# Kernel optimization log

Measured on AMD Instinct MI355X. Metric: run time of the kernel, lower is better.

The kernel has to match this reference:

```python
import jax, jax.numpy as jnp
import numpy as np
from jax import lax

# fixed differential-operator kernel bank K() from SPDE_pac (8 channels of 3x3 stencils)
_K = np.zeros((8, 3, 3), np.float32)
_K[0, 1, 1] = 1.0
_K[1, 1, 1] = 2.0
_K[2, 1, 0] = -1.0; _K[2, 1, 2] = -1.0
_K[3, 1, 1] = 2.0
_K[4, 0, 1] = -1.0; _K[4, 2, 1] = -1.0
_K[5, 0, 0] = -0.5; _K[5, 2, 2] = -0.5; _K[5, 0, 2] = 0.5; _K[5, 2, 0] = 0.5
_K[6, 1, 0] = -1.0; _K[6, 1, 2] = 1.0
_K[7, 0, 1] = 1.0; _K[7, 2, 1] = -1.0
_KMAT = jnp.asarray(_K)


def _conv(x, w):
    # 3x3 same-padded conv, no bias (torch Conv2d padding=1, bias=False)
    return lax.conv_general_dilated(x, w, (1, 1), 'SAME',
                                    dimension_numbers=('NCHW', 'OIHW', 'NCHW'))


def _softplus10(x):
    return jax.nn.softplus(10.0 * x) / 10.0


def _forward(x, conv1_w, conv2_w, conv3_w, pac_w, pac_b):
    b, t, h, w = x.shape
    # ---- encode_param_CNN ----
    p = _conv(jax.nn.relu(x), conv1_w)
    p = _conv(jax.nn.relu(p), conv2_w)
    params = _conv(p, conv3_w)                       # [b, 6t, h, w]
    # ---- decode_param_CNN (kept in [b,t,h,w] layout; H = gamma*I + v v^T per pixel) ----
    kappa = _softplus10(params[:, :t])
    m1d = params[:, t:2 * t]                         # decoder m1 -> m[:,0]
    m2d = params[:, 2 * t:3 * t]                     # decoder m2 -> m[:,1]
    gamma = _softplus10(params[:, 3 * t:4 * t])
    vx = params[:, 4 * t:5 * t]
    vy = params[:, 5 * t:6 * t]
    H11 = gamma + vx * vx
    H22 = gamma + vy * vy
    H12 = vx * vy
    # ---- SPDE_pac kernel construction ----
    # guide channels as in source: (kappa, H11, 1/H11, H22, 1/H22, H12, m[:,1], m[:,0])
    guide = jnp.stack([kappa, H11, 1.0 / H11, H22, 1.0 / H22, H12, m2d, m1d], axis=2)  # [b,t,8,h,w]
    w_ker = jnp.einsum('ide,btihw->btdehw', _KMAT, guide)   # [b,t,3,3,h,w]
    w_ker = w_ker.at[:, :, 1, 1].add(1.0)                   # w_I identity-center kernel
    # ---- pixel-adaptive conv; loop over k is independent (reads x[:,k+1]) -> vectorize over time ----
    xin = x[:, 1:]                                          # [b,t-1,h,w]
    xp = jnp.pad(xin, ((0, 0), (0, 0), (1, 1), (1, 1)))
    patches = jnp.stack([xp[:, :, d:d + h, e:e + w]
                         for d in range(3) for e in range(3)], axis=2)  # [b,t-1,9,h,w]
    wflat = w_ker[:, 1:].reshape(b, t - 1, 9, h, w)
    out = jnp.einsum('k,btkhw,btkhw->bthw', pac_w.reshape(9), wflat, patches) + pac_b[0]
    # last time slice of x_spde is never written -> zeros
    return jnp.concatenate([out, jnp.zeros((b, 1, h, w), x.dtype)], axis=1)


def setup_inputs() -> dict:
    key = jax.random.key(0)
    ks = jax.random.split(key, 6)
    b, t, h, w = 4, 10, 256, 256
    dim_ae = 32
    x = jax.random.normal(ks[0], (b, t, h, w), jnp.float32)
    conv1_w = jax.random.normal(ks[1], (dim_ae, t, 3, 3), jnp.float32) * 0.05
    conv2_w = jax.random.normal(ks[2], (2 * dim_ae, dim_ae, 3, 3), jnp.float32) * 0.05
    conv3_w = jax.random.normal(ks[3], (6 * t, 2 * dim_ae, 3, 3), jnp.float32) * 0.05
    pac_w = jax.random.normal(ks[4], (1, 1, 3, 3), jnp.float32) * 0.2
    pac_b = jax.random.normal(ks[5], (1,), jnp.float32) * 0.1
    return {"x": x, "conv1_w": conv1_w, "conv2_w": conv2_w,
            "conv3_w": conv3_w, "pac_w": pac_w, "pac_b": pac_b}


def reference(x, conv1_w, conv2_w, conv3_w, pac_w, pac_b):
    return _forward(x, conv1_w, conv2_w, conv3_w, pac_w, pac_b)
```

## Files before the change

### kernel.cpp

```cpp
#include <hip/hip_runtime.h>
#include <math.h>

#define HH 256
#define WW 256
#define HW (HH * WW)
#define TB 10
#define PSTR 260

typedef __attribute__((ext_vector_type(4))) float f32x4;
typedef __attribute__((ext_vector_type(8))) short s16x8;

__device__ __forceinline__ float sp10(float x) {
    float z = 10.0f * x;
    return (fmaxf(z, 0.0f) + log1pf(expf(-fabsf(z)))) * 0.1f;
}

__device__ __forceinline__ unsigned short f2bf(float f) {
    unsigned u = __float_as_uint(f);
    u = u + 0x7FFFu + ((u >> 16) & 1u);
    return (unsigned short)(u >> 16);
}
__device__ __forceinline__ void bsplit(float v, unsigned short& h, unsigned short& l) {
    h = f2bf(v);
    float hf = __uint_as_float(((unsigned)h) << 16);
    l = f2bf(v - hf);
}
__device__ __forceinline__ unsigned pk(unsigned short a, unsigned short b) {
    return (unsigned)a | ((unsigned)b << 16);
}
__device__ __forceinline__ void sp2(float a, float b, unsigned& uh, unsigned& ul) {
    unsigned short h1, l1, h2, l2;
    bsplit(a, h1, l1); bsplit(b, h2, l2);
    uh = pk(h1, h2); ul = pk(l1, l2);
}

__global__ __launch_bounds__(256) void prep_weights(
    const float* __restrict__ w1, const float* __restrict__ w2,
    const float* __restrict__ w3,
    float* __restrict__ wt1,
    unsigned short* __restrict__ wA2h, unsigned short* __restrict__ wA2l,
    unsigned short* __restrict__ wA3h, unsigned short* __restrict__ wA3l)
{
    int idx = blockIdx.x * 256 + threadIdx.x;
    if (idx < 2880) {
        int ci = idx / 288; int rem = idx - ci * 288;
        int tap = rem / 32; int co = rem - tap * 32;
        wt1[idx] = w1[co * 90 + ci * 9 + tap];
    }
    if (idx < 18432) {
        int t = idx / 2048; int rem = idx - t * 2048;
        int co = rem >> 5; int ci = rem & 31;
        unsigned short h, l;
        bsplit(w2[(co * 32 + ci) * 9 + t], h, l);
        wA2h[idx] = h; wA2l[idx] = l;
    }
    if (idx < 36864) {
        int t = idx / 4096; int rem = idx - t * 4096;
        int co = rem >> 6; int ci = rem & 63;
        float v = 0.0f;
        if (co < 54) {
            int tt = co / 6 + 1;
            int g  = co - (tt - 1) * 6;
            v = w3[((g * 10 + tt) * 64 + ci) * 9 + t];
        }
        unsigned short h, l;
        bsplit(v, h, l);
        wA3h[idx] = h; wA3l[idx] = l;
    }
}

__global__ __launch_bounds__(256, 4) void conv1_k(
    const float* __restrict__ x, const float* __restrict__ wt1,
    unsigned short* __restrict__ q1h, unsigned short* __restrict__ q1l)
{
    __shared__ float tile[10 * 612];
    const int tx = threadIdx.x & 15, ty = threadIdx.x >> 4;
    const int h0 = blockIdx.y * 32, w0 = blockIdx.x * 16;
    const int b = blockIdx.z;
    const float* inb = x + (size_t)b * TB * HW;

    float acc0[32], acc1[32];
#pragma unroll
    for (int c = 0; c < 32; ++c) { acc0[c] = 0.0f; acc1[c] = 0.0f; }

    for (int i = threadIdx.x; i < 10 * 612; i += 256) {
        int ci = i / 612; int r = i - ci * 612;
        int row = r / 18; int col = r - row * 18;
        int gy = h0 + row - 1, gx = w0 + col - 1;
        float v = 0.0f;
        if (gy >= 0 && gy < HH && gx >= 0 && gx < WW)
            v = fmaxf(inb[(size_t)ci * HW + gy * WW + gx], 0.0f);
        tile[i] = v;
    }
    __syncthreads();

    for (int ci = 0; ci < 10; ++ci) {
        const float* tp = &tile[ci * 612 + (2 * ty) * 18 + tx];
        float v[12];
#pragma unroll
        for (int r = 0; r < 4; ++r)
#pragma unroll
            for (int c = 0; c < 3; ++c)
                v[r * 3 + c] = tp[r * 18 + c];
        const float* wp = wt1 + ci * 288;
#pragma unroll
        for (int t = 0; t < 9; ++t) {
            float a0 = v[t], a1 = v[t + 3];
#pragma unroll
            for (int c = 0; c < 32; ++c) {
                float wv = wp[t * 32 + c];
                acc0[c] = fmaf(wv, a0, acc0[c]);
                acc1[c] = fmaf(wv, a1, acc1[c]);
            }
        }
    }

    const int h = h0 + 2 * ty, w = w0 + tx;
    const size_t q1base = (size_t)b * HW * 32;
#pragma unroll
    for (int p = 0; p < 2; ++p) {
        const float* src = p ? acc1 : acc0;
        size_t off = q1base + ((size_t)(h + p) * WW + w) * 32;
#pragma unroll
        for (int g = 0; g < 4; ++g) {
            uint4 Uh, Ul;
            sp2(fmaxf(src[g*8+0],0.f), fmaxf(src[g*8+1],0.f), Uh.x, Ul.x);
            sp2(fmaxf(src[g*8+2],0.f), fmaxf(src[g*8+3],0.f), Uh.y, Ul.y);
            sp2(fmaxf(src[g*8+4],0.f), fmaxf(src[g*8+5],0.f), Uh.z, Ul.z);
            sp2(fmaxf(src[g*8+6],0.f), fmaxf(src[g*8+7],0.f), Uh.w, Ul.w);
            *(uint4*)(q1h + off + g * 8) = Uh;
            *(uint4*)(q1l + off + g * 8) = Ul;
        }
    }
}

__global__ __launch_bounds__(256, 3) void conv2_mfma(
    const unsigned short* __restrict__ q1h, const unsigned short* __restrict__ q1l,
    const unsigned short* __restrict__ wA2h, const unsigned short* __restrict__ wA2l,
    unsigned short* __restrict__ q2h, unsigned short* __restrict__ q2l)
{
    __shared__ short lds[324 * 72];
    const int tid = threadIdx.x;
    const int lane = tid & 63, wave = tid >> 6;
    const int px = lane & 15, quad = lane >> 4;
    const int h0 = blockIdx.y * 16, w0 = blockIdx.x * 16, b = blockIdx.z;

    f32x4 acc[4][4];
#pragma unroll
    for (int r = 0; r < 4; ++r)
#pragma unroll
        for (int ct = 0; ct < 4; ++ct)
            acc[r][ct] = (f32x4){0.f, 0.f, 0.f, 0.f};

    for (int i = tid; i < 648; i += 256) {
        int plane = (i >= 324) ? 1 : 0;
        int pos = i - plane * 324;
        int row = pos / 18, col = pos - (pos / 18) * 18;
        int gy = h0 + row - 1, gx = w0 + col - 1;
        uint4 v0 = {0,0,0,0}, v1 = v0, v2 = v0, v3 = v0;
        if (gy >= 0 && gy < HH && gx >= 0 && gx < WW) {
            const uint4* gp = (const uint4*)((plane ? q1l : q1h)
                + (size_t)b * HW * 32 + ((size_t)gy * WW + gx) * 32);
            v0 = gp[0]; v1 = gp[1]; v2 = gp[2]; v3 = gp[3];
        }
        uint4* dp = (uint4*)&lds[pos * 72 + plane * 32];
        dp[0] = v0; dp[1] = v1; dp[2] = v2; dp[3] = v3;
    }
    __syncthreads();

#pragma unroll
    for (int t = 0; t < 9; ++t) {
        const int dy = t / 3, dx = t - 3 * (t / 3);
#pragma unroll
        for (int ctp = 0; ctp < 2; ++ctp) {
            const int c0 = ctp * 2;
            int wb0 = (t * 64 + (c0 + 0) * 16 + px) * 32 + quad * 8;
            int wb1 = (t * 64 + (c0 + 1) * 16 + px) * 32 + quad * 8;
            s16x8 ah0 = *(const s16x8*)(wA2h + wb0);
            s16x8 ah1 = *(const s16x8*)(wA2h + wb1);
            s16x8 al0 = *(const s16x8*)(wA2l + wb0);
            s16x8 al1 = *(const s16x8*)(wA2l + wb1);
#pragma unroll
            for (int r = 0; r < 4; ++r) {
                int py = wave * 4 + r;
                const short* bp = &lds[((py + dy) * 18 + (px + dx)) * 72 + quad * 8];
                s16x8 bh = *(const s16x8*)bp;
                s16x8 bl = *(const s16x8*)(bp + 32);
                acc[r][c0+0] = __builtin_amdgcn_mfma_f32_16x16x32_bf16(ah0, bh, acc[r][c0+0], 0, 0, 0);
                acc[r][c0+0] = __builtin_amdgcn_mfma_f32_16x16x32_bf16(al0, bh, acc[r][c0+0], 0, 0, 0);
                acc[r][c0+0] = __builtin_amdgcn_mfma_f32_16x16x32_bf16(ah0, bl, acc[r][c0+0], 0, 0, 0);
                acc[r][c0+1] = __builtin_amdgcn_mfma_f32_16x16x32_bf16(ah1, bh, acc[r][c0+1], 0, 0, 0);
                acc[r][c0+1] = __builtin_amdgcn_mfma_f32_16x16x32_bf16(al1, bh, acc[r][c0+1], 0, 0, 0);
                acc[r][c0+1] = __builtin_amdgcn_mfma_f32_16x16x32_bf16(ah1, bl, acc[r][c0+1], 0, 0, 0);
            }
        }
    }

#pragma unroll
    for (int r = 0; r < 4; ++r) {
        int py = wave * 4 + r;
        size_t pix = (size_t)b * HW + (size_t)(h0 + py) * WW + (w0 + px);
#pragma unroll
        for (int ct = 0; ct < 4; ++ct) {
            int co0 = ct * 16 + quad * 4;
            uint2 Uh, Ul;
            sp2(acc[r][ct][0], acc[r][ct][1], Uh.x, Ul.x);
            sp2(acc[r][ct][2], acc[r][ct][3], Uh.y, Ul.y);
            size_t off = pix * 64 + co0;
            *(uint2*)(q2h + off) = Uh;
            *(uint2*)(q2l + off) = Ul;
        }
    }
}

__global__ __launch_bounds__(256, 3) void conv3_mfma(
    const unsigned short* __restrict__ q2h, const unsigned short* __restrict__ q2l,
    const unsigned short* __restrict__ wA3h, const unsigned short* __restrict__ wA3l,
    const float* __restrict__ x, const float* __restrict__ pacw,
    const float* __restrict__ pacb, float* __restrict__ out)
{
    __shared__ short lds[324 * 72];
    float* smemf = (float*)lds;
    const int tid = threadIdx.x;
    const int lane = tid & 63, wave = tid >> 6;
    const int px = lane & 15, quad = lane >> 4;
    const int h0 = blockIdx.y * 16, w0 = blockIdx.x * 16, b = blockIdx.z;

    f32x4 acc[4][4];
#pragma unroll
    for (int r = 0; r < 4; ++r)
#pragma unroll
        for (int ct = 0; ct < 4; ++ct)
            acc[r][ct] = (f32x4){0.f, 0.f, 0.f, 0.f};

#pragma unroll
    for (int half = 0; half < 2; ++half) {
        if (half) __syncthreads();
        for (int i = tid; i < 648; i += 256) {
            int plane = (i >= 324) ? 1 : 0;
            int pos = i - plane * 324;
            int row = pos / 18, col = pos - (pos / 18) * 18;
            int gy = h0 + row - 1, gx = w0 + col - 1;
            uint4 v0 = {0,0,0,0}, v1 = v0, v2 = v0, v3 = v0;
            if (gy >= 0 && gy < HH && gx >= 0 && gx < WW) {
                const uint4* gp = (const uint4*)((plane ? q2l : q2h)
                    + (size_t)b * HW * 64 + ((size_t)gy * WW + gx) * 64 + half * 32);
                v0 = gp[0]; v1 = gp[1]; v2 = gp[2]; v3 = gp[3];
            }
            uint4* dp = (uint4*)&lds[pos * 72 + plane * 32];
            dp[0] = v0; dp[1] = v1; dp[2] = v2; dp[3] = v3;
        }
        __syncthreads();

#pragma unroll
        for (int t = 0; t < 9; ++t) {
            const int dy = t / 3, dx = t - 3 * (t / 3);
#pragma unroll
            for (int ctp = 0; ctp < 2; ++ctp) {
                const int c0 = ctp * 2;
                int wb0 = (t * 64 + (c0 + 0) * 16 + px) * 64 + half * 32 + quad * 8;
                int wb1 = (t * 64 + (c0 + 1) * 16 + px) * 64 + half * 32 + quad * 8;
                s16x8 ah0 = *(const s16x8*)(wA3h + wb0);
                s16x8 ah1 = *(const s16x8*)(wA3h + wb1);
                s16x8 al0 = *(const s16x8*)(wA3l + wb0);
                s16x8 al1 = *(const s16x8*)(wA3l + wb1);
#pragma unroll
                for (int r = 0; r < 4; ++r) {
                    int py = wave * 4 + r;
                    const short* bp = &lds[((py + dy) * 18 + (px + dx)) * 72 + quad * 8];
                    s16x8 bh = *(const s16x8*)bp;
                    s16x8 bl = *(const s16x8*)(bp + 32);
                    acc[r][c0+0] = __builtin_amdgcn_mfma_f32_16x16x32_bf16(ah0, bh, acc[r][c0+0], 0, 0, 0);
                    acc[r][c0+0] = __builtin_amdgcn_mfma_f32_16x16x32_bf16(al0, bh, acc[r][c0+0], 0, 0, 0);
                    acc[r][c0+0] = __builtin_amdgcn_mfma_f32_16x16x32_bf16(ah0, bl, acc[r][c0+0], 0, 0, 0);
                    acc[r][c0+1] = __builtin_amdgcn_mfma_f32_16x16x32_bf16(ah1, bh, acc[r][c0+1], 0, 0, 0);
                    acc[r][c0+1] = __builtin_amdgcn_mfma_f32_16x16x32_bf16(al1, bh, acc[r][c0+1], 0, 0, 0);
                    acc[r][c0+1] = __builtin_amdgcn_mfma_f32_16x16x32_bf16(ah1, bl, acc[r][c0+1], 0, 0, 0);
                }
            }
        }
    }

    float pw[9];
#pragma unroll
    for (int k = 0; k < 9; ++k) pw[k] = pacw[k];
    const float pbias = pacb[0];
    const int h = h0 + (tid >> 4), w = w0 + (tid & 15);
    const float* xb = x + (size_t)b * TB * HW;
    float* ob = out + (size_t)b * TB * HW;

#pragma unroll
    for (int chunk = 0; chunk < 2; ++chunk) {
        const int lo = chunk * 30, hi = chunk ? 54 : 30;
        __syncthreads();
#pragma unroll
        for (int r = 0; r < 4; ++r) {
            int pfr = (wave * 4 + r) * 16 + px;
#pragma unroll
            for (int ct = 0; ct < 4; ++ct)
#pragma unroll
                for (int g = 0; g < 4; ++g) {
                    int co = ct * 16 + quad * 4 + g;
                    if (co >= lo && co < hi)
                        smemf[(co - lo) * PSTR + pfr] = acc[r][ct][g];
                }
        }
        __syncthreads();

        const int j0 = chunk * 5, j1 = chunk ? 9 : 5;
        for (int j = j0; j < j1; ++j) {
            const int cb = j * 6 - lo;
            float kappa = sp10(smemf[(cb + 0) * PSTR + tid]);
            float m1d   = smemf[(cb + 1) * PSTR + tid];
            float m2d   = smemf[(cb + 2) * PSTR + tid];
            float gamma = sp10(smemf[(cb + 3) * PSTR + tid]);
            float vx    = smemf[(cb + 4) * PSTR + tid];
            float vy    = smemf[(cb + 5) * PSTR + tid];
            float H11 = gamma + vx * vx;
            float H22 = gamma + vy * vy;
            float H12 = vx * vy;
            float iH11 = 1.0f / H11;
            float iH22 = 1.0f / H22;
            float wk[9];
            wk[0] = -0.5f * H12;  wk[1] = -iH22 + m1d;  wk[2] = 0.5f * H12;
            wk[3] = -iH11 - m2d;
            wk[4] = kappa + 2.0f * H11 + 2.0f * H22 + 1.0f;
            wk[5] = -iH11 + m2d;
            wk[6] = 0.5f * H12;   wk[7] = -iH22 - m1d;  wk[8] = -0.5f * H12;

            const float* xc = xb + (size_t)(j + 1) * HW;
            float s = 0.0f;
#pragma unroll
            for (int dy = 0; dy < 3; ++dy)
#pragma unroll
                for (int dx = 0; dx < 3; ++dx) {
                    int gy = h + dy - 1, gx = w + dx - 1;
                    float xv = (gy >= 0 && gy < HH && gx >= 0 && gx < WW)
                                   ? xc[gy * WW + gx] : 0.0f;
                    s = fmaf(pw[dy * 3 + dx] * wk[dy * 3 + dx], xv, s);
                }
            ob[(size_t)j * HW + (size_t)h * WW + w] = s + pbias;
        }
    }
    ob[(size_t)9 * HW + (size_t)h * WW + w] = 0.0f;
}

extern "C" void kernel_launch(void* const* d_in, const int* in_sizes, int n_in,
                              void* d_out, int out_size, void* d_ws, size_t ws_size,
                              hipStream_t stream)
{
    const float* x    = (const float*)d_in[0];
    const float* w1   = (const float*)d_in[1];
    const float* w2   = (const float*)d_in[2];
    const float* w3   = (const float*)d_in[3];
    const float* pacw = (const float*)d_in[4];
    const float* pacb = (const float*)d_in[5];
    float* out = (float*)d_out;
    char* p = (char*)d_ws;

    float* wt1 = (float*)p;
    unsigned short* wA2h = (unsigned short*)(p + 11520);
    unsigned short* wA2l = (unsigned short*)(p + 11520 + 36864);
    unsigned short* wA3h = (unsigned short*)(p + 11520 + 2 * 36864);
    unsigned short* wA3l = (unsigned short*)(p + 11520 + 2 * 36864 + 73728);
    const size_t woff = 11520 + 2 * 36864 + 2 * 73728;

    prep_weights<<<144, 256, 0, stream>>>(w1, w2, w3, wt1, wA2h, wA2l, wA3h, wA3l);

    const size_t q1sz1 = (size_t)HW * 32 * 2;
    const size_t q2sz1 = (size_t)HW * 64 * 2;
    const size_t need_full = woff + 4 * (2 * q1sz1 + 2 * q2sz1);
    dim3 blk(256);

    if (ws_size >= need_full) {
        unsigned short* q1h = (unsigned short*)(p + woff);
        unsigned short* q1l = (unsigned short*)(p + woff + 4 * q1sz1);
        unsigned short* q2h = (unsigned short*)(p + woff + 8 * q1sz1);
        unsigned short* q2l = (unsigned short*)(p + woff + 8 * q1sz1 + 4 * q2sz1);
        conv1_k<<<dim3(16, 8, 4), blk, 0, stream>>>(x, wt1, q1h, q1l);
        conv2_mfma<<<dim3(16, 16, 4), blk, 0, stream>>>(q1h, q1l, wA2h, wA2l, q2h, q2l);
        conv3_mfma<<<dim3(16, 16, 4), blk, 0, stream>>>(q2h, q2l, wA3h, wA3l,
                                                        x, pacw, pacb, out);
    } else {
        unsigned short* q1h = (unsigned short*)(p + woff);
        unsigned short* q1l = (unsigned short*)(p + woff + q1sz1);
        unsigned short* q2h = (unsigned short*)(p + woff + 2 * q1sz1);
        unsigned short* q2l = (unsigned short*)(p + woff + 2 * q1sz1 + q2sz1);
        for (int b = 0; b < 4; ++b) {
            const float* xb = x + (size_t)b * TB * HW;
            float* outb = out + (size_t)b * TB * HW;
            conv1_k<<<dim3(16, 8, 1), blk, 0, stream>>>(xb, wt1, q1h, q1l);
            conv2_mfma<<<dim3(16, 16, 1), blk, 0, stream>>>(q1h, q1l, wA2h, wA2l, q2h, q2l);
            conv3_mfma<<<dim3(16, 16, 1), blk, 0, stream>>>(q2h, q2l, wA3h, wA3l,
                                                            xb, pacw, pacb, outb);
        }
    }
}
```

Before: 310.0 us.

## Split conv2/conv3 output channels across 8 waves with 512-thread blocks

```diff
diff --git a/kernel.cpp b/kernel.cpp
--- a/kernel.cpp
+++ b/kernel.cpp
@@ -134,7 +134,7 @@
     }
 }
 
-__global__ __launch_bounds__(256, 3) void conv2_mfma(
+__global__ __launch_bounds__(512, 4) void conv2_mfma(
     const unsigned short* __restrict__ q1h, const unsigned short* __restrict__ q1l,
     const unsigned short* __restrict__ wA2h, const unsigned short* __restrict__ wA2l,
     unsigned short* __restrict__ q2h, unsigned short* __restrict__ q2l)
@@ -142,17 +142,18 @@
     __shared__ short lds[324 * 72];
     const int tid = threadIdx.x;
     const int lane = tid & 63, wave = tid >> 6;
+    const int wq = wave & 3, wc = wave >> 2;
     const int px = lane & 15, quad = lane >> 4;
     const int h0 = blockIdx.y * 16, w0 = blockIdx.x * 16, b = blockIdx.z;
 
-    f32x4 acc[4][4];
+    f32x4 acc[4][2];
 #pragma unroll
     for (int r = 0; r < 4; ++r)
 #pragma unroll
-        for (int ct = 0; ct < 4; ++ct)
-            acc[r][ct] = (f32x4){0.f, 0.f, 0.f, 0.f};
-
-    for (int i = tid; i < 648; i += 256) {
+        for (int c = 0; c < 2; ++c)
+            acc[r][c] = (f32x4){0.f, 0.f, 0.f, 0.f};
+
+    for (int i = tid; i < 648; i += 512) {
         int plane = (i >= 324) ? 1 : 0;
         int pos = i - plane * 324;
         int row = pos / 18, col = pos - (pos / 18) * 18;
@@ -171,41 +172,38 @@
 #pragma unroll
     for (int t = 0; t < 9; ++t) {
         const int dy = t / 3, dx = t - 3 * (t / 3);
-#pragma unroll
-        for (int ctp = 0; ctp < 2; ++ctp) {
-            const int c0 = ctp * 2;
-            int wb0 = (t * 64 + (c0 + 0) * 16 + px) * 32 + quad * 8;
-            int wb1 = (t * 64 + (c0 + 1) * 16 + px) * 32 + quad * 8;
-            s16x8 ah0 = *(const s16x8*)(wA2h + wb0);
-            s16x8 ah1 = *(const s16x8*)(wA2h + wb1);
-            s16x8 al0 = *(const s16x8*)(wA2l + wb0);
-            s16x8 al1 = *(const s16x8*)(wA2l + wb1);
-#pragma unroll
-            for (int r = 0; r < 4; ++r) {
-                int py = wave * 4 + r;
-                const short* bp = &lds[((py + dy) * 18 + (px + dx)) * 72 + quad * 8];
-                s16x8 bh = *(const s16x8*)bp;
-                s16x8 bl = *(const s16x8*)(bp + 32);
-                acc[r][c0+0] = __builtin_amdgcn_mfma_f32_16x16x32_bf16(ah0, bh, acc[r][c0+0], 0, 0, 0);
-                acc[r][c0+0] = __builtin_amdgcn_mfma_f32_16x16x32_bf16(al0, bh, acc[r][c0+0], 0, 0, 0);
-                acc[r][c0+0] = __builtin_amdgcn_mfma_f32_16x16x32_bf16(ah0, bl, acc[r][c0+0], 0, 0, 0);
-                acc[r][c0+1] = __builtin_amdgcn_mfma_f32_16x16x32_bf16(ah1, bh, acc[r][c0+1], 0, 0, 0);
-                acc[r][c0+1] = __builtin_amdgcn_mfma_f32_16x16x32_bf16(al1, bh, acc[r][c0+1], 0, 0, 0);
-                acc[r][c0+1] = __builtin_amdgcn_mfma_f32_16x16x32_bf16(ah1, bl, acc[r][c0+1], 0, 0, 0);
-            }
+        const int ct0 = wc * 2;
+        int wb0 = (t * 64 + (ct0 + 0) * 16 + px) * 32 + quad * 8;
+        int wb1 = (t * 64 + (ct0 + 1) * 16 + px) * 32 + quad * 8;
+        s16x8 ah0 = *(const s16x8*)(wA2h + wb0);
+        s16x8 ah1 = *(const s16x8*)(wA2h + wb1);
+        s16x8 al0 = *(const s16x8*)(wA2l + wb0);
+        s16x8 al1 = *(const s16x8*)(wA2l + wb1);
+#pragma unroll
+        for (int r = 0; r < 4; ++r) {
+            int py = wq * 4 + r;
+            const short* bp = &lds[((py + dy) * 18 + (px + dx)) * 72 + quad * 8];
+            s16x8 bh = *(const s16x8*)bp;
+            s16x8 bl = *(const s16x8*)(bp + 32);
+            acc[r][0] = __builtin_amdgcn_mfma_f32_16x16x32_bf16(ah0, bh, acc[r][0], 0, 0, 0);
+            acc[r][0] = __builtin_amdgcn_mfma_f32_16x16x32_bf16(al0, bh, acc[r][0], 0, 0, 0);
+            acc[r][0] = __builtin_amdgcn_mfma_f32_16x16x32_bf16(ah0, bl, acc[r][0], 0, 0, 0);
+            acc[r][1] = __builtin_amdgcn_mfma_f32_16x16x32_bf16(ah1, bh, acc[r][1], 0, 0, 0);
+            acc[r][1] = __builtin_amdgcn_mfma_f32_16x16x32_bf16(al1, bh, acc[r][1], 0, 0, 0);
+            acc[r][1] = __builtin_amdgcn_mfma_f32_16x16x32_bf16(ah1, bl, acc[r][1], 0, 0, 0);
         }
     }
 
 #pragma unroll
     for (int r = 0; r < 4; ++r) {
-        int py = wave * 4 + r;
+        int py = wq * 4 + r;
         size_t pix = (size_t)b * HW + (size_t)(h0 + py) * WW + (w0 + px);
 #pragma unroll
-        for (int ct = 0; ct < 4; ++ct) {
-            int co0 = ct * 16 + quad * 4;
+        for (int c = 0; c < 2; ++c) {
+            int co0 = (wc * 2 + c) * 16 + quad * 4;
             uint2 Uh, Ul;
-            sp2(acc[r][ct][0], acc[r][ct][1], Uh.x, Ul.x);
-            sp2(acc[r][ct][2], acc[r][ct][3], Uh.y, Ul.y);
+            sp2(acc[r][c][0], acc[r][c][1], Uh.x, Ul.x);
+            sp2(acc[r][c][2], acc[r][c][3], Uh.y, Ul.y);
             size_t off = pix * 64 + co0;
             *(uint2*)(q2h + off) = Uh;
             *(uint2*)(q2l + off) = Ul;
@@ -213,7 +211,7 @@
     }
 }
 
-__global__ __launch_bounds__(256, 3) void conv3_mfma(
+__global__ __launch_bounds__(512, 4) void conv3_mfma(
     const unsigned short* __restrict__ q2h, const unsigned short* __restrict__ q2l,
     const unsigned short* __restrict__ wA3h, const unsigned short* __restrict__ wA3l,
     const float* __restrict__ x, const float* __restrict__ pacw,
@@ -223,20 +221,21 @@
     float* smemf = (float*)lds;
     const int tid = threadIdx.x;
     const int lane = tid & 63, wave = tid >> 6;
+    const int wq = wave & 3, wc = wave >> 2;
     const int px = lane & 15, quad = lane >> 4;
     const int h0 = blockIdx.y * 16, w0 = blockIdx.x * 16, b = blockIdx.z;
 
-    f32x4 acc[4][4];
+    f32x4 acc[4][2];
 #pragma unroll
     for (int r = 0; r < 4; ++r)
 #pragma unroll
-        for (int ct = 0; ct < 4; ++ct)
-            acc[r][ct] = (f32x4){0.f, 0.f, 0.f, 0.f};
+        for (int c = 0; c < 2; ++c)
+            acc[r][c] = (f32x4){0.f, 0.f, 0.f, 0.f};
 
 #pragma unroll
     for (int half = 0; half < 2; ++half) {
         if (half) __syncthreads();
-        for (int i = tid; i < 648; i += 256) {
+        for (int i = tid; i < 648; i += 512) {
             int plane = (i >= 324) ? 1 : 0;
             int pos = i - plane * 324;
             int row = pos / 18, col = pos - (pos / 18) * 18;
@@ -255,28 +254,25 @@
 #pragma unroll
         for (int t = 0; t < 9; ++t) {
             const int dy = t / 3, dx = t - 3 * (t / 3);
-#pragma unroll
-            for (int ctp = 0; ctp < 2; ++ctp) {
-                const int c0 = ctp * 2;
-                int wb0 = (t * 64 + (c0 + 0) * 16 + px) * 64 + half * 32 + quad * 8;
-                int wb1 = (t * 64 + (c0 + 1) * 16 + px) * 64 + half * 32 + quad * 8;
-                s16x8 ah0 = *(const s16x8*)(wA3h + wb0);
-                s16x8 ah1 = *(const s16x8*)(wA3h + wb1);
-                s16x8 al0 = *(const s16x8*)(wA3l + wb0);
-                s16x8 al1 = *(const s16x8*)(wA3l + wb1);
-#pragma unroll
-                for (int r = 0; r < 4; ++r) {
-                    int py = wave * 4 + r;
-                    const short* bp = &lds[((py + dy) * 18 + (px + dx)) * 72 + quad * 8];
-                    s16x8 bh = *(const s16x8*)bp;
-                    s16x8 bl = *(const s16x8*)(bp + 32);
-                    acc[r][c0+0] = __builtin_amdgcn_mfma_f32_16x16x32_bf16(ah0, bh, acc[r][c0+0], 0, 0, 0);
-                    acc[r][c0+0] = __builtin_amdgcn_mfma_f32_16x16x32_bf16(al0, bh, acc[r][c0+0], 0, 0, 0);
-                    acc[r][c0+0] = __builtin_amdgcn_mfma_f32_16x16x32_bf16(ah0, bl, acc[r][c0+0], 0, 0, 0);
-                    acc[r][c0+1] = __builtin_amdgcn_mfma_f32_16x16x32_bf16(ah1, bh, acc[r][c0+1], 0, 0, 0);
-                    acc[r][c0+1] = __builtin_amdgcn_mfma_f32_16x16x32_bf16(al1, bh, acc[r][c0+1], 0, 0, 0);
-                    acc[r][c0+1] = __builtin_amdgcn_mfma_f32_16x16x32_bf16(ah1, bl, acc[r][c0+1], 0, 0, 0);
-                }
+            const int ct0 = wc * 2;
+            int wb0 = (t * 64 + (ct0 + 0) * 16 + px) * 64 + half * 32 + quad * 8;
+            int wb1 = (t * 64 + (ct0 + 1) * 16 + px) * 64 + half * 32 + quad * 8;
+            s16x8 ah0 = *(const s16x8*)(wA3h + wb0);
+            s16x8 ah1 = *(const s16x8*)(wA3h + wb1);
+            s16x8 al0 = *(const s16x8*)(wA3l + wb0);
+            s16x8 al1 = *(const s16x8*)(wA3l + wb1);
+#pragma unroll
+            for (int r = 0; r < 4; ++r) {
+                int py = wq * 4 + r;
+                const short* bp = &lds[((py + dy) * 18 + (px + dx)) * 72 + quad * 8];
+                s16x8 bh = *(const s16x8*)bp;
+                s16x8 bl = *(const s16x8*)(bp + 32);
+                acc[r][0] = __builtin_amdgcn_mfma_f32_16x16x32_bf16(ah0, bh, acc[r][0], 0, 0, 0);
+                acc[r][0] = __builtin_amdgcn_mfma_f32_16x16x32_bf16(al0, bh, acc[r][0], 0, 0, 0);
+                acc[r][0] = __builtin_amdgcn_mfma_f32_16x16x32_bf16(ah0, bl, acc[r][0], 0, 0, 0);
+                acc[r][1] = __builtin_amdgcn_mfma_f32_16x16x32_bf16(ah1, bh, acc[r][1], 0, 0, 0);
+                acc[r][1] = __builtin_amdgcn_mfma_f32_16x16x32_bf16(al1, bh, acc[r][1], 0, 0, 0);
+                acc[r][1] = __builtin_amdgcn_mfma_f32_16x16x32_bf16(ah1, bl, acc[r][1], 0, 0, 0);
             }
         }
     }
@@ -285,7 +281,9 @@
 #pragma unroll
     for (int k = 0; k < 9; ++k) pw[k] = pacw[k];
     const float pbias = pacb[0];
-    const int h = h0 + (tid >> 4), w = w0 + (tid & 15);
+    const int grp = tid >> 8;
+    const int pidx = tid & 255;
+    const int h = h0 + (pidx >> 4), w = w0 + (pidx & 15);
     const float* xb = x + (size_t)b * TB * HW;
     float* ob = out + (size_t)b * TB * HW;
 
@@ -295,27 +293,28 @@
         __syncthreads();
 #pragma unroll
         for (int r = 0; r < 4; ++r) {
-            int pfr = (wave * 4 + r) * 16 + px;
-#pragma unroll
-            for (int ct = 0; ct < 4; ++ct)
+            int pfr = (wq * 4 + r) * 16 + px;
+#pragma unroll
+            for (int c = 0; c < 2; ++c)
 #pragma unroll
                 for (int g = 0; g < 4; ++g) {
-                    int co = ct * 16 + quad * 4 + g;
+                    int co = (wc * 2 + c) * 16 + quad * 4 + g;
                     if (co >= lo && co < hi)
-                        smemf[(co - lo) * PSTR + pfr] = acc[r][ct][g];
+                        smemf[(co - lo) * PSTR + pfr] = acc[r][c][g];
                 }
         }
         __syncthreads();
 
-        const int j0 = chunk * 5, j1 = chunk ? 9 : 5;
+        const int j0 = chunk ? (grp ? 7 : 5) : (grp ? 3 : 0);
+        const int j1 = chunk ? (grp ? 9 : 7) : (grp ? 5 : 3);
         for (int j = j0; j < j1; ++j) {
             const int cb = j * 6 - lo;
-            float kappa = sp10(smemf[(cb + 0) * PSTR + tid]);
-            float m1d   = smemf[(cb + 1) * PSTR + tid];
-            float m2d   = smemf[(cb + 2) * PSTR + tid];
-            float gamma = sp10(smemf[(cb + 3) * PSTR + tid]);
-            float vx    = smemf[(cb + 4) * PSTR + tid];
-            float vy    = smemf[(cb + 5) * PSTR + tid];
+            float kappa = sp10(smemf[(cb + 0) * PSTR + pidx]);
+            float m1d   = smemf[(cb + 1) * PSTR + pidx];
+            float m2d   = smemf[(cb + 2) * PSTR + pidx];
+            float gamma = sp10(smemf[(cb + 3) * PSTR + pidx]);
+            float vx    = smemf[(cb + 4) * PSTR + pidx];
+            float vy    = smemf[(cb + 5) * PSTR + pidx];
             float H11 = gamma + vx * vx;
             float H22 = gamma + vy * vy;
             float H12 = vx * vy;
@@ -342,7 +341,8 @@
             ob[(size_t)j * HW + (size_t)h * WW + w] = s + pbias;
         }
     }
-    ob[(size_t)9 * HW + (size_t)h * WW + w] = 0.0f;
+    if (grp == 0)
+        ob[(size_t)9 * HW + (size_t)h * WW + w] = 0.0f;
 }
 
 extern "C" void kernel_launch(void* const* d_in, const int* in_sizes, int n_in,
@@ -370,17 +370,16 @@
     const size_t q1sz1 = (size_t)HW * 32 * 2;
     const size_t q2sz1 = (size_t)HW * 64 * 2;
     const size_t need_full = woff + 4 * (2 * q1sz1 + 2 * q2sz1);
-    dim3 blk(256);
 
     if (ws_size >= need_full) {
         unsigned short* q1h = (unsigned short*)(p + woff);
         unsigned short* q1l = (unsigned short*)(p + woff + 4 * q1sz1);
         unsigned short* q2h = (unsigned short*)(p + woff + 8 * q1sz1);
         unsigned short* q2l = (unsigned short*)(p + woff + 8 * q1sz1 + 4 * q2sz1);
-        conv1_k<<<dim3(16, 8, 4), blk, 0, stream>>>(x, wt1, q1h, q1l);
-        conv2_mfma<<<dim3(16, 16, 4), blk, 0, stream>>>(q1h, q1l, wA2h, wA2l, q2h, q2l);
-        conv3_mfma<<<dim3(16, 16, 4), blk, 0, stream>>>(q2h, q2l, wA3h, wA3l,
-                                                        x, pacw, pacb, out);
+        conv1_k<<<dim3(16, 8, 4), dim3(256), 0, stream>>>(x, wt1, q1h, q1l);
+        conv2_mfma<<<dim3(16, 16, 4), dim3(512), 0, stream>>>(q1h, q1l, wA2h, wA2l, q2h, q2l);
+        conv3_mfma<<<dim3(16, 16, 4), dim3(512), 0, stream>>>(q2h, q2l, wA3h, wA3l,
+                                                              x, pacw, pacb, out);
     } else {
         unsigned short* q1h = (unsigned short*)(p + woff);
         unsigned short* q1l = (unsigned short*)(p + woff + q1sz1);
@@ -389,10 +388,10 @@
         for (int b = 0; b < 4; ++b) {
             const float* xb = x + (size_t)b * TB * HW;
             float* outb = out + (size_t)b * TB * HW;
-            conv1_k<<<dim3(16, 8, 1), blk, 0, stream>>>(xb, wt1, q1h, q1l);
-            conv2_mfma<<<dim3(16, 16, 1), blk, 0, stream>>>(q1h, q1l, wA2h, wA2l, q2h, q2l);
-            conv3_mfma<<<dim3(16, 16, 1), blk, 0, stream>>>(q2h, q2l, wA3h, wA3l,
-                                                            xb, pacw, pacb, outb);
-        }
-    }
-}
+            conv1_k<<<dim3(16, 8, 1), dim3(256), 0, stream>>>(xb, wt1, q1h, q1l);
+            conv2_mfma<<<dim3(16, 16, 1), dim3(512), 0, stream>>>(q1h, q1l, wA2h, wA2l, q2h, q2l);
+            conv3_mfma<<<dim3(16, 16, 1), dim3(512), 0, stream>>>(q2h, q2l, wA3h, wA3l,
+                                                                  xb, pacw, pacb, outb);
+        }
+    }
+}
```

After: 278.2 us. -10.3%, faster.

## Split conv2/conv3 output channels across two blocks to double grid size

Applied to the files above, without the earlier changes.

```diff
diff --git a/kernel.cpp b/kernel.cpp
--- a/kernel.cpp
+++ b/kernel.cpp
@@ -32,6 +32,11 @@
     unsigned short h1, l1, h2, l2;
     bsplit(a, h1, l1); bsplit(b, h2, l2);
     uh = pk(h1, h2); ul = pk(l1, l2);
+}
+
+template <int NB> __device__ __forceinline__ int log2nb() {
+    static_assert(NB == 1 || NB == 2 || NB == 4, "NB pow2");
+    return NB == 4 ? 2 : (NB == 2 ? 1 : 0);
 }
 
 __global__ __launch_bounds__(256) void prep_weights(
@@ -134,7 +139,8 @@
     }
 }
 
-__global__ __launch_bounds__(256, 3) void conv2_mfma(
+template <int NB>
+__global__ __launch_bounds__(256) void conv2_mfma(
     const unsigned short* __restrict__ q1h, const unsigned short* __restrict__ q1l,
     const unsigned short* __restrict__ wA2h, const unsigned short* __restrict__ wA2l,
     unsigned short* __restrict__ q2h, unsigned short* __restrict__ q2l)
@@ -143,14 +149,17 @@
     const int tid = threadIdx.x;
     const int lane = tid & 63, wave = tid >> 6;
     const int px = lane & 15, quad = lane >> 4;
-    const int h0 = blockIdx.y * 16, w0 = blockIdx.x * 16, b = blockIdx.z;
-
-    f32x4 acc[4][4];
+    const int z = blockIdx.z;
+    const int b = z & (NB - 1);
+    const int cohalf = z >> log2nb<NB>();
+    const int h0 = blockIdx.y * 16, w0 = blockIdx.x * 16;
+
+    f32x4 acc[4][2];
 #pragma unroll
     for (int r = 0; r < 4; ++r)
 #pragma unroll
-        for (int ct = 0; ct < 4; ++ct)
-            acc[r][ct] = (f32x4){0.f, 0.f, 0.f, 0.f};
+        for (int c = 0; c < 2; ++c)
+            acc[r][c] = (f32x4){0.f, 0.f, 0.f, 0.f};
 
     for (int i = tid; i < 648; i += 256) {
         int plane = (i >= 324) ? 1 : 0;
@@ -171,27 +180,24 @@
 #pragma unroll
     for (int t = 0; t < 9; ++t) {
         const int dy = t / 3, dx = t - 3 * (t / 3);
-#pragma unroll
-        for (int ctp = 0; ctp < 2; ++ctp) {
-            const int c0 = ctp * 2;
-            int wb0 = (t * 64 + (c0 + 0) * 16 + px) * 32 + quad * 8;
-            int wb1 = (t * 64 + (c0 + 1) * 16 + px) * 32 + quad * 8;
-            s16x8 ah0 = *(const s16x8*)(wA2h + wb0);
-            s16x8 ah1 = *(const s16x8*)(wA2h + wb1);
-            s16x8 al0 = *(const s16x8*)(wA2l + wb0);
-            s16x8 al1 = *(const s16x8*)(wA2l + wb1);
-#pragma unroll
-            for (int r = 0; r < 4; ++r) {
-                int py = wave * 4 + r;
-                const short* bp = &lds[((py + dy) * 18 + (px + dx)) * 72 + quad * 8];
-                s16x8 bh = *(const s16x8*)bp;
-                s16x8 bl = *(const s16x8*)(bp + 32);
-                acc[r][c0+0] = __builtin_amdgcn_mfma_f32_16x16x32_bf16(ah0, bh, acc[r][c0+0], 0, 0, 0);
-                acc[r][c0+0] = __builtin_amdgcn_mfma_f32_16x16x32_bf16(al0, bh, acc[r][c0+0], 0, 0, 0);
-                acc[r][c0+0] = __builtin_amdgcn_mfma_f32_16x16x32_bf16(ah0, bl, acc[r][c0+0], 0, 0, 0);
-                acc[r][c0+1] = __builtin_amdgcn_mfma_f32_16x16x32_bf16(ah1, bh, acc[r][c0+1], 0, 0, 0);
-                acc[r][c0+1] = __builtin_amdgcn_mfma_f32_16x16x32_bf16(al1, bh, acc[r][c0+1], 0, 0, 0);
-                acc[r][c0+1] = __builtin_amdgcn_mfma_f32_16x16x32_bf16(ah1, bl, acc[r][c0+1], 0, 0, 0);
+        s16x8 ah[2], al[2];
+#pragma unroll
+        for (int ct = 0; ct < 2; ++ct) {
+            int wb = (t * 64 + cohalf * 32 + ct * 16 + px) * 32 + quad * 8;
+            ah[ct] = *(const s16x8*)(wA2h + wb);
+            al[ct] = *(const s16x8*)(wA2l + wb);
+        }
+#pragma unroll
+        for (int r = 0; r < 4; ++r) {
+            int py = wave * 4 + r;
+            const short* bp = &lds[((py + dy) * 18 + (px + dx)) * 72 + quad * 8];
+            s16x8 bh = *(const s16x8*)bp;
+            s16x8 bl = *(const s16x8*)(bp + 32);
+#pragma unroll
+            for (int ct = 0; ct < 2; ++ct) {
+                acc[r][ct] = __builtin_amdgcn_mfma_f32_16x16x32_bf16(ah[ct], bh, acc[r][ct], 0, 0, 0);
+                acc[r][ct] = __builtin_amdgcn_mfma_f32_16x16x32_bf16(al[ct], bh, acc[r][ct], 0, 0, 0);
+                acc[r][ct] = __builtin_amdgcn_mfma_f32_16x16x32_bf16(ah[ct], bl, acc[r][ct], 0, 0, 0);
             }
         }
     }
@@ -201,8 +207,8 @@
         int py = wave * 4 + r;
         size_t pix = (size_t)b * HW + (size_t)(h0 + py) * WW + (w0 + px);
 #pragma unroll
-        for (int ct = 0; ct < 4; ++ct) {
-            int co0 = ct * 16 + quad * 4;
+        for (int ct = 0; ct < 2; ++ct) {
+            int co0 = cohalf * 32 + ct * 16 + quad * 4;
             uint2 Uh, Ul;
             sp2(acc[r][ct][0], acc[r][ct][1], Uh.x, Ul.x);
             sp2(acc[r][ct][2], acc[r][ct][3], Uh.y, Ul.y);
@@ -213,7 +219,8 @@
     }
 }
 
-__global__ __launch_bounds__(256, 3) void conv3_mfma(
+template <int NB>
+__global__ __launch_bounds__(256) void conv3_mfma(
     const unsigned short* __restrict__ q2h, const unsigned short* __restrict__ q2l,
     const unsigned short* __restrict__ wA3h, const unsigned short* __restrict__ wA3l,
     const float* __restrict__ x, const float* __restrict__ pacw,
@@ -224,18 +231,22 @@
     const int tid = threadIdx.x;
     const int lane = tid & 63, wave = tid >> 6;
     const int px = lane & 15, quad = lane >> 4;
-    const int h0 = blockIdx.y * 16, w0 = blockIdx.x * 16, b = blockIdx.z;
-
-    f32x4 acc[4][4];
+    const int z = blockIdx.z;
+    const int b = z & (NB - 1);
+    const int cohalf = z >> log2nb<NB>();
+    const int base = cohalf * 24;
+    const int h0 = blockIdx.y * 16, w0 = blockIdx.x * 16;
+
+    f32x4 acc[4][2];
 #pragma unroll
     for (int r = 0; r < 4; ++r)
 #pragma unroll
-        for (int ct = 0; ct < 4; ++ct)
-            acc[r][ct] = (f32x4){0.f, 0.f, 0.f, 0.f};
-
-#pragma unroll
-    for (int half = 0; half < 2; ++half) {
-        if (half) __syncthreads();
+        for (int c = 0; c < 2; ++c)
+            acc[r][c] = (f32x4){0.f, 0.f, 0.f, 0.f};
+
+#pragma unroll
+    for (int khalf = 0; khalf < 2; ++khalf) {
+        if (khalf) __syncthreads();
         for (int i = tid; i < 648; i += 256) {
             int plane = (i >= 324) ? 1 : 0;
             int pos = i - plane * 324;
@@ -244,7 +255,7 @@
             uint4 v0 = {0,0,0,0}, v1 = v0, v2 = v0, v3 = v0;
             if (gy >= 0 && gy < HH && gx >= 0 && gx < WW) {
                 const uint4* gp = (const uint4*)((plane ? q2l : q2h)
-                    + (size_t)b * HW * 64 + ((size_t)gy * WW + gx) * 64 + half * 32);
+                    + (size_t)b * HW * 64 + ((size_t)gy * WW + gx) * 64 + khalf * 32);
                 v0 = gp[0]; v1 = gp[1]; v2 = gp[2]; v3 = gp[3];
             }
             uint4* dp = (uint4*)&lds[pos * 72 + plane * 32];
@@ -255,31 +266,43 @@
 #pragma unroll
         for (int t = 0; t < 9; ++t) {
             const int dy = t / 3, dx = t - 3 * (t / 3);
-#pragma unroll
-            for (int ctp = 0; ctp < 2; ++ctp) {
-                const int c0 = ctp * 2;
-                int wb0 = (t * 64 + (c0 + 0) * 16 + px) * 64 + half * 32 + quad * 8;
-                int wb1 = (t * 64 + (c0 + 1) * 16 + px) * 64 + half * 32 + quad * 8;
-                s16x8 ah0 = *(const s16x8*)(wA3h + wb0);
-                s16x8 ah1 = *(const s16x8*)(wA3h + wb1);
-                s16x8 al0 = *(const s16x8*)(wA3l + wb0);
-                s16x8 al1 = *(const s16x8*)(wA3l + wb1);
-#pragma unroll
-                for (int r = 0; r < 4; ++r) {
-                    int py = wave * 4 + r;
-                    const short* bp = &lds[((py + dy) * 18 + (px + dx)) * 72 + quad * 8];
-                    s16x8 bh = *(const s16x8*)bp;
-                    s16x8 bl = *(const s16x8*)(bp + 32);
-                    acc[r][c0+0] = __builtin_amdgcn_mfma_f32_16x16x32_bf16(ah0, bh, acc[r][c0+0], 0, 0, 0);
-                    acc[r][c0+0] = __builtin_amdgcn_mfma_f32_16x16x32_bf16(al0, bh, acc[r][c0+0], 0, 0, 0);
-                    acc[r][c0+0] = __builtin_amdgcn_mfma_f32_16x16x32_bf16(ah0, bl, acc[r][c0+0], 0, 0, 0);
-                    acc[r][c0+1] = __builtin_amdgcn_mfma_f32_16x16x32_bf16(ah1, bh, acc[r][c0+1], 0, 0, 0);
-                    acc[r][c0+1] = __builtin_amdgcn_mfma_f32_16x16x32_bf16(al1, bh, acc[r][c0+1], 0, 0, 0);
-                    acc[r][c0+1] = __builtin_amdgcn_mfma_f32_16x16x32_bf16(ah1, bl, acc[r][c0+1], 0, 0, 0);
+            s16x8 ah[2], al[2];
+#pragma unroll
+            for (int ct = 0; ct < 2; ++ct) {
+                int wb = (t * 64 + base + ct * 16 + px) * 64 + khalf * 32 + quad * 8;
+                ah[ct] = *(const s16x8*)(wA3h + wb);
+                al[ct] = *(const s16x8*)(wA3l + wb);
+            }
+#pragma unroll
+            for (int r = 0; r < 4; ++r) {
+                int py = wave * 4 + r;
+                const short* bp = &lds[((py + dy) * 18 + (px + dx)) * 72 + quad * 8];
+                s16x8 bh = *(const s16x8*)bp;
+                s16x8 bl = *(const s16x8*)(bp + 32);
+#pragma unroll
+                for (int ct = 0; ct < 2; ++ct) {
+                    acc[r][ct] = __builtin_amdgcn_mfma_f32_16x16x32_bf16(ah[ct], bh, acc[r][ct], 0, 0, 0);
+                    acc[r][ct] = __builtin_amdgcn_mfma_f32_16x16x32_bf16(al[ct], bh, acc[r][ct], 0, 0, 0);
+                    acc[r][ct] = __builtin_amdgcn_mfma_f32_16x16x32_bf16(ah[ct], bl, acc[r][ct], 0, 0, 0);
                 }
             }
         }
     }
+
+    __syncthreads();
+#pragma unroll
+    for (int r = 0; r < 4; ++r) {
+        int pfr = (wave * 4 + r) * 16 + px;
+#pragma unroll
+        for (int ct = 0; ct < 2; ++ct)
+#pragma unroll
+            for (int g = 0; g < 4; ++g) {
+                int slot = ct * 16 + quad * 4 + g;
+                if (slot < 30)
+                    smemf[slot * PSTR + pfr] = acc[r][ct][g];
+            }
+    }
+    __syncthreads();
 
     float pw[9];
 #pragma unroll
@@ -290,59 +313,42 @@
     float* ob = out + (size_t)b * TB * HW;
 
 #pragma unroll
-    for (int chunk = 0; chunk < 2; ++chunk) {
-        const int lo = chunk * 30, hi = chunk ? 54 : 30;
-        __syncthreads();
-#pragma unroll
-        for (int r = 0; r < 4; ++r) {
-            int pfr = (wave * 4 + r) * 16 + px;
-#pragma unroll
-            for (int ct = 0; ct < 4; ++ct)
-#pragma unroll
-                for (int g = 0; g < 4; ++g) {
-                    int co = ct * 16 + quad * 4 + g;
-                    if (co >= lo && co < hi)
-                        smemf[(co - lo) * PSTR + pfr] = acc[r][ct][g];
-                }
-        }
-        __syncthreads();
-
-        const int j0 = chunk * 5, j1 = chunk ? 9 : 5;
-        for (int j = j0; j < j1; ++j) {
-            const int cb = j * 6 - lo;
-            float kappa = sp10(smemf[(cb + 0) * PSTR + tid]);
-            float m1d   = smemf[(cb + 1) * PSTR + tid];
-            float m2d   = smemf[(cb + 2) * PSTR + tid];
-            float gamma = sp10(smemf[(cb + 3) * PSTR + tid]);
-            float vx    = smemf[(cb + 4) * PSTR + tid];
-            float vy    = smemf[(cb + 5) * PSTR + tid];
-            float H11 = gamma + vx * vx;
-            float H22 = gamma + vy * vy;
-            float H12 = vx * vy;
-            float iH11 = 1.0f / H11;
-            float iH22 = 1.0f / H22;
-            float wk[9];
-            wk[0] = -0.5f * H12;  wk[1] = -iH22 + m1d;  wk[2] = 0.5f * H12;
-            wk[3] = -iH11 - m2d;
-            wk[4] = kappa + 2.0f * H11 + 2.0f * H22 + 1.0f;
-            wk[5] = -iH11 + m2d;
-            wk[6] = 0.5f * H12;   wk[7] = -iH22 - m1d;  wk[8] = -0.5f * H12;
-
-            const float* xc = xb + (size_t)(j + 1) * HW;
-            float s = 0.0f;
-#pragma unroll
-            for (int dy = 0; dy < 3; ++dy)
-#pragma unroll
-                for (int dx = 0; dx < 3; ++dx) {
-                    int gy = h + dy - 1, gx = w + dx - 1;
-                    float xv = (gy >= 0 && gy < HH && gx >= 0 && gx < WW)
-                                   ? xc[gy * WW + gx] : 0.0f;
-                    s = fmaf(pw[dy * 3 + dx] * wk[dy * 3 + dx], xv, s);
-                }
-            ob[(size_t)j * HW + (size_t)h * WW + w] = s + pbias;
-        }
-    }
-    ob[(size_t)9 * HW + (size_t)h * WW + w] = 0.0f;
+    for (int k = 0; k < 5; ++k) {
+        const int j = cohalf * 4 + k;
+        const int cb = k * 6;
+        float kappa = sp10(smemf[(cb + 0) * PSTR + tid]);
+        float m1d   = smemf[(cb + 1) * PSTR + tid];
+        float m2d   = smemf[(cb + 2) * PSTR + tid];
+        float gamma = sp10(smemf[(cb + 3) * PSTR + tid]);
+        float vx    = smemf[(cb + 4) * PSTR + tid];
+        float vy    = smemf[(cb + 5) * PSTR + tid];
+        float H11 = gamma + vx * vx;
+        float H22 = gamma + vy * vy;
+        float H12 = vx * vy;
+        float iH11 = 1.0f / H11;
+        float iH22 = 1.0f / H22;
+        float wk[9];
+        wk[0] = -0.5f * H12;  wk[1] = -iH22 + m1d;  wk[2] = 0.5f * H12;
+        wk[3] = -iH11 - m2d;
+        wk[4] = kappa + 2.0f * H11 + 2.0f * H22 + 1.0f;
+        wk[5] = -iH11 + m2d;
+        wk[6] = 0.5f * H12;   wk[7] = -iH22 - m1d;  wk[8] = -0.5f * H12;
+
+        const float* xc = xb + (size_t)(j + 1) * HW;
+        float s = 0.0f;
+#pragma unroll
+        for (int dy = 0; dy < 3; ++dy)
+#pragma unroll
+            for (int dx = 0; dx < 3; ++dx) {
+                int gy = h + dy - 1, gx = w + dx - 1;
+                float xv = (gy >= 0 && gy < HH && gx >= 0 && gx < WW)
+                               ? xc[gy * WW + gx] : 0.0f;
+                s = fmaf(pw[dy * 3 + dx] * wk[dy * 3 + dx], xv, s);
+            }
+        ob[(size_t)j * HW + (size_t)h * WW + w] = s + pbias;
+    }
+    if (cohalf)
+        ob[(size_t)9 * HW + (size_t)h * WW + w] = 0.0f;
 }
 
 extern "C" void kernel_launch(void* const* d_in, const int* in_sizes, int n_in,
@@ -378,9 +384,9 @@
         unsigned short* q2h = (unsigned short*)(p + woff + 8 * q1sz1);
         unsigned short* q2l = (unsigned short*)(p + woff + 8 * q1sz1 + 4 * q2sz1);
         conv1_k<<<dim3(16, 8, 4), blk, 0, stream>>>(x, wt1, q1h, q1l);
-        conv2_mfma<<<dim3(16, 16, 4), blk, 0, stream>>>(q1h, q1l, wA2h, wA2l, q2h, q2l);
-        conv3_mfma<<<dim3(16, 16, 4), blk, 0, stream>>>(q2h, q2l, wA3h, wA3l,
-                                                        x, pacw, pacb, out);
+        conv2_mfma<4><<<dim3(16, 16, 8), blk, 0, stream>>>(q1h, q1l, wA2h, wA2l, q2h, q2l);
+        conv3_mfma<4><<<dim3(16, 16, 8), blk, 0, stream>>>(q2h, q2l, wA3h, wA3l,
+                                                           x, pacw, pacb, out);
     } else {
         unsigned short* q1h = (unsigned short*)(p + woff);
         unsigned short* q1l = (unsigned short*)(p + woff + q1sz1);
@@ -390,9 +396,9 @@
             const float* xb = x + (size_t)b * TB * HW;
             float* outb = out + (size_t)b * TB * HW;
             conv1_k<<<dim3(16, 8, 1), blk, 0, stream>>>(xb, wt1, q1h, q1l);
-            conv2_mfma<<<dim3(16, 16, 1), blk, 0, stream>>>(q1h, q1l, wA2h, wA2l, q2h, q2l);
-            conv3_mfma<<<dim3(16, 16, 1), blk, 0, stream>>>(q2h, q2l, wA3h, wA3l,
-                                                            xb, pacw, pacb, outb);
-        }
-    }
-}
+            conv2_mfma<1><<<dim3(16, 16, 2), blk, 0, stream>>>(q1h, q1l, wA2h, wA2l, q2h, q2l);
+            conv3_mfma<1><<<dim3(16, 16, 2), blk, 0, stream>>>(q2h, q2l, wA3h, wA3l,
+                                                               xb, pacw, pacb, outb);
+        }
+    }
+}
```

Result: faster. 265.6 us (-14.3%).
